# Kernel optimization log

Measured on AMD Instinct MI355X. Metric: run time of the kernel, lower is better.

The kernel has to match this reference:

```python
import jax, jax.numpy as jnp
import numpy as np


def setup_inputs() -> dict:
    key = jax.random.key(0)
    ks = jax.random.split(key, 4)
    B, H, W, C = 4, 64, 64, 256
    Ck = C // 8
    x = jax.random.normal(ks[0], (B, H, W, C), dtype=jnp.float32)
    Wf = jax.random.normal(ks[1], (C, Ck), dtype=jnp.float32) * (1.0 / np.sqrt(C))
    Wg = jax.random.normal(ks[2], (C, Ck), dtype=jnp.float32) * (1.0 / np.sqrt(C))
    Wh = jax.random.normal(ks[3], (C, C), dtype=jnp.float32) * (1.0 / np.sqrt(C))
    bf = jnp.zeros((Ck,), jnp.float32)
    bg = jnp.zeros((Ck,), jnp.float32)
    bh = jnp.zeros((C,), jnp.float32)
    gamma = jnp.ones((1,), jnp.float32)
    return {"x": x, "Wf": Wf, "bf": bf, "Wg": Wg, "bg": bg, "Wh": Wh, "bh": bh, "gamma": gamma}


def reference(x, Wf, bf, Wg, bg, Wh, bh, gamma):
    B, H, W, C = x.shape
    N = H * W
    xf = x.reshape(B, N, C)  # hw_flatten; 1x1 conv == per-pixel matmul
    f = xf @ Wf + bf          # [B, N, C//8] (keys)
    g = xf @ Wg + bg          # [B, N, C//8] (queries)
    h = xf @ Wh + bh          # [B, N, C]    (values)
    s = jnp.einsum('bnk,bmk->bnm', g, f)   # [B, N, N], no scaling (as in source)
    b = jax.nn.softmax(s, axis=-1)
    o = jnp.einsum('bnm,bmc->bnc', b, h)   # [B, N, C]
    y = gamma * o.reshape(B, H, W, C) + x
    return y
```

## Files before the change

### kernel.cpp

```cpp
#include <hip/hip_runtime.h>
#include <stdint.h>

typedef short short8 __attribute__((ext_vector_type(8)));
typedef short short4_t __attribute__((ext_vector_type(4)));
typedef float f32x4 __attribute__((ext_vector_type(4)));

__device__ __forceinline__ float bf2f(unsigned short u) {
    union { unsigned int i; float f; } v; v.i = ((unsigned int)u) << 16; return v.f;
}
__device__ __forceinline__ unsigned short f2bf(float f) {
    union { float f; unsigned int i; } v; v.f = f;
    return (unsigned short)((v.i + 0x8000u) >> 16);
}

__global__ __launch_bounds__(256) void k_prep(const float* __restrict__ x,
                                              unsigned short* __restrict__ xh,
                                              unsigned short* __restrict__ xl) {
    int gid = blockIdx.x * 256 + threadIdx.x;
    const float* src = x + (size_t)gid * 8;
    f32x4 a0 = *(const f32x4*)src;
    f32x4 a1 = *(const f32x4*)(src + 4);
    short8 sh, sl;
#pragma unroll
    for (int j = 0; j < 4; ++j) {
        unsigned short h0 = f2bf(a0[j]);
        sh[j] = (short)h0; sl[j] = (short)f2bf(a0[j] - bf2f(h0));
        unsigned short h1 = f2bf(a1[j]);
        sh[4 + j] = (short)h1; sl[4 + j] = (short)f2bf(a1[j] - bf2f(h1));
    }
    *(short8*)&xh[(size_t)gid * 8] = sh;
    *(short8*)&xl[(size_t)gid * 8] = sl;
}

__global__ void k_wtrans(const float* __restrict__ Wf,
                         const float* __restrict__ Wg,
                         const float* __restrict__ Wh,
                         unsigned short* __restrict__ wTh,
                         unsigned short* __restrict__ wTl) {
    int col = blockIdx.x;
    int k = threadIdx.x;
    float v;
    if (col < 32) v = Wf[k * 32 + col];
    else if (col < 64) v = Wg[k * 32 + (col - 32)];
    else v = Wh[k * 256 + (col - 64)];
    unsigned short h = f2bf(v);
    wTh[col * 256 + k] = h;
    if (col < 64) wTl[col * 256 + k] = f2bf(v - bf2f(h));
}

__global__ __launch_bounds__(256) void k_proj(
    const unsigned short* __restrict__ xh,
    const unsigned short* __restrict__ xl,
    const unsigned short* __restrict__ wTh,
    const unsigned short* __restrict__ wTl,
    const float* __restrict__ bfb,
    const float* __restrict__ bgb,
    const float* __restrict__ bhb,
    unsigned short* __restrict__ fKh,
    unsigned short* __restrict__ fKl,
    unsigned short* __restrict__ gQh,
    unsigned short* __restrict__ gQl,
    unsigned short* __restrict__ hT) {
    __shared__ short sm[4 * 64 * 72];
    int tid = threadIdx.x;
    int wave = tid >> 6, lane = tid & 63, lq = lane & 15, quad = lane >> 4;
    int rt = blockIdx.x;
    const unsigned short* xhb = xh + (size_t)rt * 64 * 256;
    const unsigned short* xlb = xl + (size_t)rt * 64 * 256;
    f32x4 zero4 = {0.f, 0.f, 0.f, 0.f};

    if (blockIdx.y < 4) {
        const int XO = 0, WO = 64 * 136;
        int cb = blockIdx.y;
        const unsigned short* wbase = wTh + (size_t)(64 + cb * 64) * 256;
        f32x4 acc[4] = {zero4, zero4, zero4, zero4};

        for (int ph = 0; ph < 2; ++ph) {
            int k0 = ph * 128;
            __syncthreads();
#pragma unroll
            for (int u = 0; u < 4; ++u) {
                int q = u * 256 + tid;
                int row = q >> 4, kc = q & 15;
                *(short8*)&sm[XO + row * 136 + kc * 8] =
                    *(const short8*)&xhb[row * 256 + k0 + kc * 8];
                *(short8*)&sm[WO + row * 136 + kc * 8] =
                    *(const short8*)&wbase[row * 256 + k0 + kc * 8];
            }
            __syncthreads();
#pragma unroll
            for (int ks = 0; ks < 4; ++ks) {
                short8 a = *(const short8*)&sm[XO + (wave * 16 + lq) * 136 + ks * 32 + quad * 8];
#pragma unroll
                for (int ct = 0; ct < 4; ++ct) {
                    short8 bfr = *(const short8*)&sm[WO + (lq + 16 * ct) * 136 + ks * 32 + quad * 8];
                    acc[ct] = __builtin_amdgcn_mfma_f32_16x16x32_bf16(a, bfr, acc[ct], 0, 0, 0);
                }
            }
        }

        int rowl = wave * 16 + quad * 4;
        int grow0 = rt * 64;
        int bidx = grow0 >> 12, n0 = (grow0 & 4095) + rowl;
#pragma unroll
        for (int ct = 0; ct < 4; ++ct) {
            int c = cb * 64 + lq + 16 * ct;
            float bias = bhb[c];
            short4_t pk;
#pragma unroll
            for (int r = 0; r < 4; ++r) pk[r] = (short)f2bf(acc[ct][r] + bias);
            *(short4_t*)&hT[((size_t)(bidx * 256 + c)) * 4096 + n0] = pk;
        }
    } else {
        const int XH = 0, XL = 64 * 72, WH = 2 * 64 * 72, WL = 3 * 64 * 72;
        f32x4 acc[4] = {zero4, zero4, zero4, zero4};

        for (int ph = 0; ph < 4; ++ph) {
            int k0 = ph * 64;
            __syncthreads();
#pragma unroll
            for (int u = 0; u < 2; ++u) {
                int q = u * 256 + tid;
                int row = q >> 3, kc = q & 7;
                *(short8*)&sm[XH + row * 72 + kc * 8] =
                    *(const short8*)&xhb[row * 256 + k0 + kc * 8];
                *(short8*)&sm[XL + row * 72 + kc * 8] =
                    *(const short8*)&xlb[row * 256 + k0 + kc * 8];
                *(short8*)&sm[WH + row * 72 + kc * 8] =
                    *(const short8*)&wTh[row * 256 + k0 + kc * 8];
                *(short8*)&sm[WL + row * 72 + kc * 8] =
                    *(const short8*)&wTl[row * 256 + k0 + kc * 8];
            }
            __syncthreads();
#pragma unroll
            for (int ks = 0; ks < 2; ++ks) {
                short8 ah = *(const short8*)&sm[XH + (wave * 16 + lq) * 72 + ks * 32 + quad * 8];
                short8 al = *(const short8*)&sm[XL + (wave * 16 + lq) * 72 + ks * 32 + quad * 8];
#pragma unroll
                for (int ct = 0; ct < 4; ++ct) {
                    short8 bh = *(const short8*)&sm[WH + (lq + 16 * ct) * 72 + ks * 32 + quad * 8];
                    short8 bl = *(const short8*)&sm[WL + (lq + 16 * ct) * 72 + ks * 32 + quad * 8];
                    acc[ct] = __builtin_amdgcn_mfma_f32_16x16x32_bf16(ah, bh, acc[ct], 0, 0, 0);
                    acc[ct] = __builtin_amdgcn_mfma_f32_16x16x32_bf16(al, bh, acc[ct], 0, 0, 0);
                    acc[ct] = __builtin_amdgcn_mfma_f32_16x16x32_bf16(ah, bl, acc[ct], 0, 0, 0);
                }
            }
        }

        int rowl = wave * 16 + quad * 4;
#pragma unroll
        for (int ct = 0; ct < 4; ++ct) {
            int coll = lq + 16 * ct;
#pragma unroll
            for (int r = 0; r < 4; ++r) {
                int grow = rt * 64 + rowl + r;
                int bidx = grow >> 12, n = grow & 4095;
                float v = acc[ct][r];
                size_t o = (size_t)(bidx * 4096 + n) * 32;
                if (coll < 32) {
                    v += bfb[coll];
                    unsigned short h = f2bf(v);
                    fKh[o + coll] = h;
                    fKl[o + coll] = f2bf(v - bf2f(h));
                } else {
                    v += bgb[coll - 32];
                    unsigned short h = f2bf(v);
                    gQh[o + (coll - 32)] = h;
                    gQl[o + (coll - 32)] = f2bf(v - bf2f(h));
                }
            }
        }
    }
}

#define PSTR 72
#define FSTR 40
__global__ __launch_bounds__(512, 2) void k_attn(
    const unsigned short* __restrict__ fKh,
    const unsigned short* __restrict__ fKl,
    const unsigned short* __restrict__ gQh,
    const unsigned short* __restrict__ gQl,
    const unsigned short* __restrict__ hT,
    float* __restrict__ pacc0,
    float* __restrict__ pacc1,
    float* __restrict__ pl0,
    float* __restrict__ pl1) {
    __shared__ short Ps[2][128 * PSTR];
    __shared__ short Fb[2][2][64 * FSTR];
    int tid = threadIdx.x;
    int wave = tid >> 6, lane = tid & 63, lq = lane & 15, quad = lane >> 4;
    int b = blockIdx.x & 3;
    int rest = blockIdx.x >> 2;
    int qt = rest & 31;
    int ks = rest >> 5;

    const unsigned short* fhB = fKh + (size_t)b * 4096 * 32;
    const unsigned short* flB = fKl + (size_t)b * 4096 * 32;
    const unsigned short* hB  = hT + (size_t)b * 256 * 4096;
    float* pacc = ks ? pacc1 : pacc0;
    float* pl   = ks ? pl1 : pl0;

    int qrow0 = qt * 128 + wave * 16;

    f32x4 zero4 = {0.f, 0.f, 0.f, 0.f};
    f32x4 acc[16];
#pragma unroll
    for (int i = 0; i < 16; ++i) acc[i] = zero4;
    float l_part[4] = {0.f, 0.f, 0.f, 0.f};

    size_t go = ((size_t)(b * 4096 + qrow0 + lq)) * 32 + quad * 8;
    short8 ghfrag = *(const short8*)&gQh[go];
    short8 glfrag = *(const short8*)&gQl[go];

    int half = tid >> 8, tt = tid & 255;
    int frow = tt >> 2, fkc = tt & 3;
    const unsigned short* fsrc = half ? flB : fhB;

    int kb0 = ks * 2048;
    *(short8*)&Fb[0][half][frow * FSTR + fkc * 8] =
        *(const short8*)&fsrc[(size_t)(kb0 + frow) * 32 + fkc * 8];
    __syncthreads();

    for (int kt = 0; kt < 32; ++kt) {
        int p = kt & 1;
        int kbase = kb0 + kt * 64;
        int nkb = kbase + 64; if (nkb > 4032) nkb = 4032;

        short8 fnext = *(const short8*)&fsrc[(size_t)(nkb + frow) * 32 + fkc * 8];

        short8 hb0[2], hb1[2];
#pragma unroll
        for (int ct = 0; ct < 2; ++ct) {
            const unsigned short* hp =
                hB + (size_t)(wave * 32 + ct * 16 + lq) * 4096 + kbase + quad * 8;
            hb0[ct] = *(const short8*)hp;
            hb1[ct] = *(const short8*)(hp + 32);
        }

        f32x4 S[4];
#pragma unroll
        for (int t = 0; t < 4; ++t) {
            short8 fh = *(const short8*)&Fb[p][0][(lq + 16 * t) * FSTR + quad * 8];
            short8 fl = *(const short8*)&Fb[p][1][(lq + 16 * t) * FSTR + quad * 8];
            S[t] = __builtin_amdgcn_mfma_f32_16x16x32_bf16(ghfrag, fh, zero4, 0, 0, 0);
            S[t] = __builtin_amdgcn_mfma_f32_16x16x32_bf16(glfrag, fh, S[t], 0, 0, 0);
            S[t] = __builtin_amdgcn_mfma_f32_16x16x32_bf16(ghfrag, fl, S[t], 0, 0, 0);
        }

#pragma unroll
        for (int t = 0; t < 4; ++t)
#pragma unroll
            for (int r = 0; r < 4; ++r) S[t][r] = __expf(S[t][r]);
#pragma unroll
        for (int r = 0; r < 4; ++r)
            l_part[r] += (S[0][r] + S[1][r]) + (S[2][r] + S[3][r]);

#pragma unroll
        for (int t = 0; t < 4; ++t)
#pragma unroll
            for (int r = 0; r < 4; ++r)
                Ps[p][(wave * 16 + quad * 4 + r) * PSTR + lq + 16 * t] =
                    (short)f2bf(S[t][r]);

        *(short8*)&Fb[1 - p][half][frow * FSTR + fkc * 8] = fnext;

        __syncthreads();

#pragma unroll
        for (int rb = 0; rb < 8; ++rb) {
            short8 pa0 = *(const short8*)&Ps[p][(rb * 16 + lq) * PSTR + quad * 8];
            short8 pa1 = *(const short8*)&Ps[p][(rb * 16 + lq) * PSTR + 32 + quad * 8];
#pragma unroll
            for (int ct = 0; ct < 2; ++ct) {
                acc[rb * 2 + ct] = __builtin_amdgcn_mfma_f32_16x16x32_bf16(pa0, hb0[ct], acc[rb * 2 + ct], 0, 0, 0);
                acc[rb * 2 + ct] = __builtin_amdgcn_mfma_f32_16x16x32_bf16(pa1, hb1[ct], acc[rb * 2 + ct], 0, 0, 0);
            }
        }
    }

#pragma unroll
    for (int r = 0; r < 4; ++r) {
        float s = l_part[r];
        s += __shfl_xor(s, 1);
        s += __shfl_xor(s, 2);
        s += __shfl_xor(s, 4);
        s += __shfl_xor(s, 8);
        if (lq == 0)
            pl[b * 4096 + qrow0 + quad * 4 + r] = s;
    }
#pragma unroll
    for (int rb = 0; rb < 8; ++rb)
#pragma unroll
        for (int ct = 0; ct < 2; ++ct) {
            int c = wave * 32 + ct * 16 + lq;
#pragma unroll
            for (int r = 0; r < 4; ++r) {
                int n = qt * 128 + rb * 16 + quad * 4 + r;
                pacc[((size_t)(b * 4096 + n)) * 256 + c] = acc[rb * 2 + ct][r];
            }
        }
}

__global__ __launch_bounds__(256) void k_combine(
    const float* __restrict__ x,
    const float* __restrict__ gam_p,
    const float* __restrict__ pacc1,
    const float* __restrict__ pl0,
    const float* __restrict__ pl1,
    float* __restrict__ out) {
    int gid = blockIdx.x * 256 + threadIdx.x;
    int row = gid >> 6;
    f32x4 a0 = *(const f32x4*)&out[(size_t)gid * 4];
    f32x4 a1 = *(const f32x4*)&pacc1[(size_t)gid * 4];
    f32x4 xv = *(const f32x4*)&x[(size_t)gid * 4];
    float linv = 1.0f / (pl0[row] + pl1[row]);
    float gam = gam_p[0];
    f32x4 o;
#pragma unroll
    for (int j = 0; j < 4; ++j) o[j] = gam * ((a0[j] + a1[j]) * linv) + xv[j];
    *(f32x4*)&out[(size_t)gid * 4] = o;
}

extern "C" void kernel_launch(void* const* d_in, const int* in_sizes, int n_in,
                              void* d_out, int out_size, void* d_ws, size_t ws_size,
                              hipStream_t stream) {
    const float* x   = (const float*)d_in[0];
    const float* Wf  = (const float*)d_in[1];
    const float* bfb = (const float*)d_in[2];
    const float* Wg  = (const float*)d_in[3];
    const float* bgb = (const float*)d_in[4];
    const float* Wh  = (const float*)d_in[5];
    const float* bhb = (const float*)d_in[6];
    const float* gam = (const float*)d_in[7];
    float* out = (float*)d_out;

    char* ws = (char*)d_ws;
    const size_t MI = 1u << 20;
    unsigned short* xh  = (unsigned short*)(ws);
    unsigned short* xl  = (unsigned short*)(ws + 8 * MI);
    unsigned short* fKh = (unsigned short*)(ws + 16 * MI);
    unsigned short* fKl = (unsigned short*)(ws + 17 * MI);
    unsigned short* gQh = (unsigned short*)(ws + 18 * MI);
    unsigned short* gQl = (unsigned short*)(ws + 19 * MI);
    unsigned short* hT  = (unsigned short*)(ws + 20 * MI);
    unsigned short* wTh = (unsigned short*)(ws + 28 * MI);
    unsigned short* wTl = (unsigned short*)(ws + 28 * MI + 160 * 1024);
    float* pacc1 = (float*)(ws + 29 * MI);
    float* pl0   = (float*)(ws + 45 * MI);
    float* pl1   = (float*)(ws + 45 * MI + 64 * 1024);

    k_prep<<<dim3(2048), dim3(256), 0, stream>>>(x, xh, xl);
    k_wtrans<<<dim3(320), dim3(256), 0, stream>>>(Wf, Wg, Wh, wTh, wTl);
    k_proj<<<dim3(256, 5), dim3(256), 0, stream>>>(xh, xl, wTh, wTl, bfb, bgb, bhb,
                                                   fKh, fKl, gQh, gQl, hT);
    k_attn<<<dim3(256), dim3(512), 0, stream>>>(fKh, fKl, gQh, gQl, hT,
                                                out, pacc1, pl0, pl1);
    k_combine<<<dim3(4096), dim3(256), 0, stream>>>(x, gam, pacc1, pl0, pl1, out);
}
```

Before: 170.5 us.

## Pre-swizzle K/Q/V into MFMA fragment layout and retile attention to 64-row blocks

The projection kernel now writes f, g and transposed h directly in MFMA fragment-tiled order, so the attention kernel can load whole contiguous 16-row tiles with one short8 per thread and no padded strided LDS staging. The attention kernel is retiled from 128 query rows and 8 waves to 64 rows and 4 waves per block, with each wave owning 64 output channels, and launches twice as many blocks. The x-prep and weight-transpose kernels are merged into one launch. This is meant to cut scattered global loads and LDS bank conflicts, but it doubles the reads of h per query row, and the scattered scalar stores in the projection may get more expensive.

```diff
diff --git a/kernel.cpp b/kernel.cpp
--- a/kernel.cpp
+++ b/kernel.cpp
@@ -13,39 +13,40 @@
     return (unsigned short)((v.i + 0x8000u) >> 16);
 }
 
-__global__ __launch_bounds__(256) void k_prep(const float* __restrict__ x,
-                                              unsigned short* __restrict__ xh,
-                                              unsigned short* __restrict__ xl) {
-    int gid = blockIdx.x * 256 + threadIdx.x;
-    const float* src = x + (size_t)gid * 8;
-    f32x4 a0 = *(const f32x4*)src;
-    f32x4 a1 = *(const f32x4*)(src + 4);
-    short8 sh, sl;
-#pragma unroll
-    for (int j = 0; j < 4; ++j) {
-        unsigned short h0 = f2bf(a0[j]);
-        sh[j] = (short)h0; sl[j] = (short)f2bf(a0[j] - bf2f(h0));
-        unsigned short h1 = f2bf(a1[j]);
-        sh[4 + j] = (short)h1; sl[4 + j] = (short)f2bf(a1[j] - bf2f(h1));
+__global__ __launch_bounds__(256) void k_pre(const float* __restrict__ x,
+                                             const float* __restrict__ Wf,
+                                             const float* __restrict__ Wg,
+                                             const float* __restrict__ Wh,
+                                             unsigned short* __restrict__ xh,
+                                             unsigned short* __restrict__ xl,
+                                             unsigned short* __restrict__ wTh,
+                                             unsigned short* __restrict__ wTl) {
+    if (blockIdx.x < 2048) {
+        int gid = blockIdx.x * 256 + threadIdx.x;
+        const float* src = x + (size_t)gid * 8;
+        f32x4 a0 = *(const f32x4*)src;
+        f32x4 a1 = *(const f32x4*)(src + 4);
+        short8 sh, sl;
+#pragma unroll
+        for (int j = 0; j < 4; ++j) {
+            unsigned short h0 = f2bf(a0[j]);
+            sh[j] = (short)h0; sl[j] = (short)f2bf(a0[j] - bf2f(h0));
+            unsigned short h1 = f2bf(a1[j]);
+            sh[4 + j] = (short)h1; sl[4 + j] = (short)f2bf(a1[j] - bf2f(h1));
+        }
+        *(short8*)&xh[(size_t)gid * 8] = sh;
+        *(short8*)&xl[(size_t)gid * 8] = sl;
+    } else {
+        int col = blockIdx.x - 2048;
+        int k = threadIdx.x;
+        float v;
+        if (col < 32) v = Wf[k * 32 + col];
+        else if (col < 64) v = Wg[k * 32 + (col - 32)];
+        else v = Wh[k * 256 + (col - 64)];
+        unsigned short h = f2bf(v);
+        wTh[col * 256 + k] = h;
+        if (col < 64) wTl[col * 256 + k] = f2bf(v - bf2f(h));
     }
-    *(short8*)&xh[(size_t)gid * 8] = sh;
-    *(short8*)&xl[(size_t)gid * 8] = sl;
-}
-
-__global__ void k_wtrans(const float* __restrict__ Wf,
-                         const float* __restrict__ Wg,
-                         const float* __restrict__ Wh,
-                         unsigned short* __restrict__ wTh,
-                         unsigned short* __restrict__ wTl) {
-    int col = blockIdx.x;
-    int k = threadIdx.x;
-    float v;
-    if (col < 32) v = Wf[k * 32 + col];
-    else if (col < 64) v = Wg[k * 32 + (col - 32)];
-    else v = Wh[k * 256 + (col - 64)];
-    unsigned short h = f2bf(v);
-    wTh[col * 256 + k] = h;
-    if (col < 64) wTl[col * 256 + k] = f2bf(v - bf2f(h));
 }
 
 __global__ __launch_bounds__(256) void k_proj(
@@ -109,7 +110,9 @@
             short4_t pk;
 #pragma unroll
             for (int r = 0; r < 4; ++r) pk[r] = (short)f2bf(acc[ct][r] + bias);
-            *(short4_t*)&hT[((size_t)(bidx * 256 + c)) * 4096 + n0] = pk;
+            size_t a8 = (((size_t)(bidx * 16 + (c >> 4)) * 128 + (n0 >> 5)) * 64 +
+                         ((n0 & 31) >> 3) * 16 + (c & 15)) * 8 + (n0 & 7);
+            *(short4_t*)&hT[a8] = pk;
         }
     } else {
         const int XH = 0, XL = 64 * 72, WH = 2 * 64 * 72, WL = 3 * 64 * 72;
@@ -156,17 +159,21 @@
                 int grow = rt * 64 + rowl + r;
                 int bidx = grow >> 12, n = grow & 4095;
                 float v = acc[ct][r];
-                size_t o = (size_t)(bidx * 4096 + n) * 32;
+                size_t o = (size_t)(bidx * 256 + (n >> 4)) * 512 +
+                           (((coll & 31) >> 3) * 16 + (n & 15)) * 8 + (coll & 7);
                 if (coll < 32) {
                     v += bfb[coll];
                     unsigned short h = f2bf(v);
-                    fKh[o + coll] = h;
-                    fKl[o + coll] = f2bf(v - bf2f(h));
+                    fKh[o] = h;
+                    fKl[o] = f2bf(v - bf2f(h));
                 } else {
-                    v += bgb[coll - 32];
+                    int cg = coll - 32;
+                    size_t og = (size_t)(bidx * 256 + (n >> 4)) * 512 +
+                                ((cg >> 3) * 16 + (n & 15)) * 8 + (cg & 7);
+                    v += bgb[cg];
                     unsigned short h = f2bf(v);
-                    gQh[o + (coll - 32)] = h;
-                    gQl[o + (coll - 32)] = f2bf(v - bf2f(h));
+                    gQh[og] = h;
+                    gQl[og] = f2bf(v - bf2f(h));
                 }
             }
         }
@@ -174,8 +181,7 @@
 }
 
 #define PSTR 72
-#define FSTR 40
-__global__ __launch_bounds__(512, 2) void k_attn(
+__global__ __launch_bounds__(256, 2) void k_attn(
     const unsigned short* __restrict__ fKh,
     const unsigned short* __restrict__ fKl,
     const unsigned short* __restrict__ gQh,
@@ -185,22 +191,23 @@
     float* __restrict__ pacc1,
     float* __restrict__ pl0,
     float* __restrict__ pl1) {
-    __shared__ short Ps[2][128 * PSTR];
-    __shared__ short Fb[2][2][64 * FSTR];
+    __shared__ short Ps[2][64 * PSTR];
+    __shared__ short Fb[2][2][2048];
     int tid = threadIdx.x;
     int wave = tid >> 6, lane = tid & 63, lq = lane & 15, quad = lane >> 4;
     int b = blockIdx.x & 3;
     int rest = blockIdx.x >> 2;
-    int qt = rest & 31;
-    int ks = rest >> 5;
-
-    const unsigned short* fhB = fKh + (size_t)b * 4096 * 32;
-    const unsigned short* flB = fKl + (size_t)b * 4096 * 32;
-    const unsigned short* hB  = hT + (size_t)b * 256 * 4096;
+    int qt = rest & 63;
+    int ks = rest >> 6;
+
+    const unsigned short* fhB = fKh + (size_t)b * 131072;
+    const unsigned short* flB = fKl + (size_t)b * 131072;
+    const unsigned short* hB  = hT + (size_t)b * 1048576;
     float* pacc = ks ? pacc1 : pacc0;
     float* pl   = ks ? pl1 : pl0;
 
-    int qrow0 = qt * 128 + wave * 16;
+    int qrow0 = qt * 64 + wave * 16;
+    int lchunk = quad * 16 + lq;
 
     f32x4 zero4 = {0.f, 0.f, 0.f, 0.f};
     f32x4 acc[16];
@@ -208,40 +215,37 @@
     for (int i = 0; i < 16; ++i) acc[i] = zero4;
     float l_part[4] = {0.f, 0.f, 0.f, 0.f};
 
-    size_t go = ((size_t)(b * 4096 + qrow0 + lq)) * 32 + quad * 8;
-    short8 ghfrag = *(const short8*)&gQh[go];
-    short8 glfrag = *(const short8*)&gQl[go];
-
-    int half = tid >> 8, tt = tid & 255;
-    int frow = tt >> 2, fkc = tt & 3;
-    const unsigned short* fsrc = half ? flB : fhB;
-
-    int kb0 = ks * 2048;
-    *(short8*)&Fb[0][half][frow * FSTR + fkc * 8] =
-        *(const short8*)&fsrc[(size_t)(kb0 + frow) * 32 + fkc * 8];
+    int gtile = b * 256 + qt * 4 + wave;
+    short8 ghfrag = *(const short8*)&gQh[(size_t)gtile * 512 + lchunk * 8];
+    short8 glfrag = *(const short8*)&gQl[(size_t)gtile * 512 + lchunk * 8];
+
+    int ft0 = ks * 128;
+    *(short8*)&Fb[0][0][tid * 8] = *(const short8*)&fhB[(size_t)ft0 * 512 + tid * 8];
+    *(short8*)&Fb[0][1][tid * 8] = *(const short8*)&flB[(size_t)ft0 * 512 + tid * 8];
     __syncthreads();
 
     for (int kt = 0; kt < 32; ++kt) {
         int p = kt & 1;
-        int kbase = kb0 + kt * 64;
-        int nkb = kbase + 64; if (nkb > 4032) nkb = 4032;
-
-        short8 fnext = *(const short8*)&fsrc[(size_t)(nkb + frow) * 32 + fkc * 8];
-
-        short8 hb0[2], hb1[2];
-#pragma unroll
-        for (int ct = 0; ct < 2; ++ct) {
-            const unsigned short* hp =
-                hB + (size_t)(wave * 32 + ct * 16 + lq) * 4096 + kbase + quad * 8;
-            hb0[ct] = *(const short8*)hp;
-            hb1[ct] = *(const short8*)(hp + 32);
+        int nft = ft0 + (kt < 31 ? (kt + 1) * 4 : kt * 4);
+        short8 fnh = *(const short8*)&fhB[(size_t)nft * 512 + tid * 8];
+        short8 fnl = *(const short8*)&flB[(size_t)nft * 512 + tid * 8];
+
+        int k0 = ks * 64 + kt * 2;
+        short8 hb[4][2];
+#pragma unroll
+        for (int ct = 0; ct < 4; ++ct) {
+            int ctile = wave * 4 + ct;
+#pragma unroll
+            for (int kk = 0; kk < 2; ++kk)
+                hb[ct][kk] = *(const short8*)
+                    &hB[(((size_t)ctile * 128 + k0 + kk) * 64 + lchunk) * 8];
         }
 
         f32x4 S[4];
 #pragma unroll
         for (int t = 0; t < 4; ++t) {
-            short8 fh = *(const short8*)&Fb[p][0][(lq + 16 * t) * FSTR + quad * 8];
-            short8 fl = *(const short8*)&Fb[p][1][(lq + 16 * t) * FSTR + quad * 8];
+            short8 fh = *(const short8*)&Fb[p][0][t * 512 + lchunk * 8];
+            short8 fl = *(const short8*)&Fb[p][1][t * 512 + lchunk * 8];
             S[t] = __builtin_amdgcn_mfma_f32_16x16x32_bf16(ghfrag, fh, zero4, 0, 0, 0);
             S[t] = __builtin_amdgcn_mfma_f32_16x16x32_bf16(glfrag, fh, S[t], 0, 0, 0);
             S[t] = __builtin_amdgcn_mfma_f32_16x16x32_bf16(ghfrag, fl, S[t], 0, 0, 0);
@@ -262,18 +266,19 @@
                 Ps[p][(wave * 16 + quad * 4 + r) * PSTR + lq + 16 * t] =
                     (short)f2bf(S[t][r]);
 
-        *(short8*)&Fb[1 - p][half][frow * FSTR + fkc * 8] = fnext;
+        *(short8*)&Fb[1 - p][0][tid * 8] = fnh;
+        *(short8*)&Fb[1 - p][1][tid * 8] = fnl;
 
         __syncthreads();
 
 #pragma unroll
-        for (int rb = 0; rb < 8; ++rb) {
+        for (int rb = 0; rb < 4; ++rb) {
             short8 pa0 = *(const short8*)&Ps[p][(rb * 16 + lq) * PSTR + quad * 8];
             short8 pa1 = *(const short8*)&Ps[p][(rb * 16 + lq) * PSTR + 32 + quad * 8];
 #pragma unroll
-            for (int ct = 0; ct < 2; ++ct) {
-                acc[rb * 2 + ct] = __builtin_amdgcn_mfma_f32_16x16x32_bf16(pa0, hb0[ct], acc[rb * 2 + ct], 0, 0, 0);
-                acc[rb * 2 + ct] = __builtin_amdgcn_mfma_f32_16x16x32_bf16(pa1, hb1[ct], acc[rb * 2 + ct], 0, 0, 0);
+            for (int ct = 0; ct < 4; ++ct) {
+                acc[rb * 4 + ct] = __builtin_amdgcn_mfma_f32_16x16x32_bf16(pa0, hb[ct][0], acc[rb * 4 + ct], 0, 0, 0);
+                acc[rb * 4 + ct] = __builtin_amdgcn_mfma_f32_16x16x32_bf16(pa1, hb[ct][1], acc[rb * 4 + ct], 0, 0, 0);
             }
         }
     }
@@ -289,14 +294,14 @@
             pl[b * 4096 + qrow0 + quad * 4 + r] = s;
     }
 #pragma unroll
-    for (int rb = 0; rb < 8; ++rb)
-#pragma unroll
-        for (int ct = 0; ct < 2; ++ct) {
-            int c = wave * 32 + ct * 16 + lq;
+    for (int rb = 0; rb < 4; ++rb)
+#pragma unroll
+        for (int ct = 0; ct < 4; ++ct) {
+            int c = wave * 64 + ct * 16 + lq;
 #pragma unroll
             for (int r = 0; r < 4; ++r) {
-                int n = qt * 128 + rb * 16 + quad * 4 + r;
-                pacc[((size_t)(b * 4096 + n)) * 256 + c] = acc[rb * 2 + ct][r];
+                int n = qt * 64 + rb * 16 + quad * 4 + r;
+                pacc[((size_t)(b * 4096 + n)) * 256 + c] = acc[rb * 4 + ct][r];
             }
         }
 }
@@ -349,11 +354,10 @@
     float* pl0   = (float*)(ws + 45 * MI);
     float* pl1   = (float*)(ws + 45 * MI + 64 * 1024);
 
-    k_prep<<<dim3(2048), dim3(256), 0, stream>>>(x, xh, xl);
-    k_wtrans<<<dim3(320), dim3(256), 0, stream>>>(Wf, Wg, Wh, wTh, wTl);
+    k_pre<<<dim3(2368), dim3(256), 0, stream>>>(x, Wf, Wg, Wh, xh, xl, wTh, wTl);
     k_proj<<<dim3(256, 5), dim3(256), 0, stream>>>(xh, xl, wTh, wTl, bfb, bgb, bhb,
                                                    fKh, fKl, gQh, gQl, hT);
-    k_attn<<<dim3(256), dim3(512), 0, stream>>>(fKh, fKl, gQh, gQl, hT,
+    k_attn<<<dim3(512), dim3(256), 0, stream>>>(fKh, fKl, gQh, gQl, hT,
                                                 out, pacc1, pl0, pl1);
     k_combine<<<dim3(4096), dim3(256), 0, stream>>>(x, gam, pacc1, pl0, pl1, out);
 }
```

Measured after the change: 154.1 us. -9.7%, faster.
